# Performance work log

Measured on AMD Instinct MI355X. Metric: run time of the kernel, lower is better.

## Reference

```python
import jax, jax.numpy as jnp
import numpy as np

B, TQ, TK = 2, 2048, 2048
D_IN, D_OUT, H = 1024, 1024, 16
HD = D_OUT // H  # head dim = 64


def setup_inputs() -> dict:
    key = jax.random.key(0)
    ks = jax.random.split(key, 11)
    s = 1.0 / np.sqrt(D_IN)
    so = 1.0 / np.sqrt(D_OUT)
    return {
        "q": jax.random.normal(ks[0], (B, TQ, D_IN), jnp.float32),
        "k": jax.random.normal(ks[1], (B, TK, D_IN), jnp.float32),
        "v": jax.random.normal(ks[2], (B, TK, D_IN), jnp.float32),
        "Wq": jax.random.uniform(ks[3], (D_OUT, D_IN), jnp.float32, -s, s),
        "bq": jax.random.uniform(ks[4], (D_OUT,), jnp.float32, -s, s),
        "Wk": jax.random.uniform(ks[5], (D_OUT, D_IN), jnp.float32, -s, s),
        "bk": jax.random.uniform(ks[6], (D_OUT,), jnp.float32, -s, s),
        "Wv": jax.random.uniform(ks[7], (D_OUT, D_IN), jnp.float32, -s, s),
        "bv": jax.random.uniform(ks[8], (D_OUT,), jnp.float32, -s, s),
        "Wo": jax.random.uniform(ks[9], (D_OUT, D_OUT), jnp.float32, -so, so),
        "bo": jax.random.uniform(ks[10], (D_OUT,), jnp.float32, -so, so),
    }


def reference(q, k, v, Wq, bq, Wk, bk, Wv, bv, Wo, bo):
    b, tq, _ = q.shape
    tk = k.shape[1]
    # linear projections, split heads: [B,T,D] -> [B,H,T,HD]
    qh = (q @ Wq.T + bq).reshape(b, tq, H, HD).transpose(0, 2, 1, 3)
    kh = (k @ Wk.T + bk).reshape(b, tk, H, HD).transpose(0, 2, 1, 3)
    vh = (v @ Wv.T + bv).reshape(b, tk, H, HD).transpose(0, 2, 1, 3)
    # scaled dot-product attention (forward never applies the causal mask)
    scores = jnp.einsum("bhqd,bhkd->bhqk", qh, kh) / np.sqrt(HD).astype(np.float32)
    attn = jax.nn.softmax(scores, axis=-1)
    x = jnp.einsum("bhqk,bhkd->bhqd", attn, vh)
    x = x.transpose(0, 2, 1, 3).reshape(b, tq, D_OUT)
    return x @ Wo.T + bo
```

## Files before the change

kernel.cpp:

```cpp
#include <hip/hip_runtime.h>
#include <hip/hip_bf16.h>

typedef __bf16 b16x8 __attribute__((ext_vector_type(8)));
typedef unsigned short u16x8 __attribute__((ext_vector_type(8)));
typedef unsigned short u16x4 __attribute__((ext_vector_type(4)));
typedef unsigned int u32x4 __attribute__((ext_vector_type(4)));
typedef unsigned int u32x2 __attribute__((ext_vector_type(2)));
typedef float f32x4 __attribute__((ext_vector_type(4)));
typedef float f32x16 __attribute__((ext_vector_type(16)));

__device__ __forceinline__ unsigned short f2b(float f) {
  unsigned u = __builtin_bit_cast(unsigned, f);
  u += 0x7fff + ((u >> 16) & 1);
  return (unsigned short)(u >> 16);
}

__device__ __forceinline__ b16x8 as_b(u16x8 v) { return __builtin_bit_cast(b16x8, v); }

__device__ __forceinline__ float fexp2(float x) {
#if __has_builtin(__builtin_amdgcn_exp2f)
  return __builtin_amdgcn_exp2f(x);
#else
  return exp2f(x);
#endif
}

__device__ __forceinline__ unsigned cvtpk(float lo, float hi) {
  unsigned r;
  asm("v_cvt_pk_bf16_f32 %0, %1, %2" : "=v"(r) : "v"(lo), "v"(hi));
  return r;
}

__device__ __forceinline__ void plswap(unsigned& a, unsigned& b) {
  asm volatile("v_permlane32_swap_b32 %0, %1" : "+v"(a), "+v"(b));
}

__device__ __forceinline__ b16x8 mkchunk(float p0, float p1, float p2, float p3,
                                         float p4, float p5, float p6, float p7) {
  unsigned a1 = cvtpk(p0, p1), b1 = cvtpk(p4, p5);
  unsigned a2 = cvtpk(p2, p3), b2 = cvtpk(p6, p7);
  plswap(a1, b1);
  plswap(a2, b2);
  u32x4 w = {a1, a2, b1, b2};
  return __builtin_bit_cast(b16x8, w);
}

#define AS1 __attribute__((address_space(1)))
#define AS3 __attribute__((address_space(3)))
__device__ __forceinline__ void gload_lds16(const void* g, void* l) {
  __builtin_amdgcn_global_load_lds((const AS1 void*)g, (AS3 void*)l, 16, 0, 0);
}


__global__ __launch_bounds__(256) void convert_kernel(
    const float* __restrict__ q, const float* __restrict__ k, const float* __restrict__ v,
    const float* __restrict__ Wq, const float* __restrict__ Wk,
    const float* __restrict__ Wv, const float* __restrict__ Wo,
    unsigned short* __restrict__ qb, unsigned short* __restrict__ kb,
    unsigned short* __restrict__ vb, unsigned short* __restrict__ wqb,
    unsigned short* __restrict__ wkb, unsigned short* __restrict__ wvb,
    unsigned short* __restrict__ wob) {
  const float* src; unsigned short* dst; int rows;
  switch (blockIdx.y) {
    case 0: src = q;  dst = qb;  rows = 4096; break;
    case 1: src = k;  dst = kb;  rows = 4096; break;
    case 2: src = v;  dst = vb;  rows = 4096; break;
    case 3: src = Wq; dst = wqb; rows = 1024; break;
    case 4: src = Wk; dst = wkb; rows = 1024; break;
    case 5: src = Wv; dst = wvb; rows = 1024; break;
    default: src = Wo; dst = wob; rows = 1024; break;
  }
  const int row = blockIdx.x * 2 + (threadIdx.x >> 7);
  if (row >= rows) return;
  const int t = threadIdx.x & 127;
  const float* sp = src + (size_t)row * 1024 + t * 8;
  float4 f0 = *(const float4*)sp;
  float4 f1 = *(const float4*)(sp + 4);
  u16x8 h = { f2b(f0.x), f2b(f0.y), f2b(f0.z), f2b(f0.w),
              f2b(f1.x), f2b(f1.y), f2b(f1.z), f2b(f1.w) };
  const int swcol = ((t >> 3) << 6) | (((t & 7) ^ (row & 7)) << 3);
  *(u16x8*)(dst + (size_t)row * 1024 + swcol) = h;
}

template <int MODE, typename TOUT>
__device__ __forceinline__ void gemm_body(unsigned short* sA, unsigned short* sB,
                                          const unsigned short* __restrict__ A,
                                          const unsigned short* __restrict__ Bm,
                                          const float* __restrict__ bias,
                                          TOUT* __restrict__ C) {
  const int tid = threadIdx.x;
  const int l = tid & 63, w = tid >> 6;
  const int wm = w >> 1, wn = w & 1;
  const int lr = l & 15, lg = l >> 4;
  const int bm = blockIdx.y * 64, bn = blockIdx.x * 128;
  const int r8 = l >> 3, sl = l & 7;

  f32x4 acc[2][4] = {};

  for (int k0 = 0; k0 < 1024; k0 += 64) {
#pragma unroll
    for (int i = 0; i < 2; ++i) {
      const int row = i * 32 + w * 8 + r8;
      gload_lds16(A + (size_t)(bm + row) * 1024 + k0 + sl * 8, &sA[i * 2048 + w * 512]);
    }
#pragma unroll
    for (int i = 0; i < 4; ++i) {
      const int row = i * 32 + w * 8 + r8;
      gload_lds16(Bm + (size_t)(bn + row) * 1024 + k0 + sl * 8, &sB[i * 2048 + w * 512]);
    }
    __syncthreads();

    b16x8 af[2][2], bf[4][2];
#pragma unroll
    for (int mb = 0; mb < 2; ++mb)
#pragma unroll
      for (int kh = 0; kh < 2; ++kh) {
        const int r = wm * 32 + mb * 16 + lr;
        af[mb][kh] = as_b(*(const u16x8*)(&sA[(r * 64 + kh * 32 + lg * 8) ^ ((r & 7) << 3)]));
      }
#pragma unroll
    for (int nb = 0; nb < 4; ++nb)
#pragma unroll
      for (int kh = 0; kh < 2; ++kh) {
        const int r = wn * 64 + nb * 16 + lr;
        bf[nb][kh] = as_b(*(const u16x8*)(&sB[(r * 64 + kh * 32 + lg * 8) ^ ((r & 7) << 3)]));
      }
#pragma unroll
    for (int mb = 0; mb < 2; ++mb)
#pragma unroll
      for (int nb = 0; nb < 4; ++nb) {
        acc[mb][nb] = __builtin_amdgcn_mfma_f32_16x16x32_bf16(af[mb][0], bf[nb][0], acc[mb][nb], 0, 0, 0);
        acc[mb][nb] = __builtin_amdgcn_mfma_f32_16x16x32_bf16(af[mb][1], bf[nb][1], acc[mb][nb], 0, 0, 0);
      }
    __syncthreads();
  }

  const float qscale = 0.125f * 1.44269504f;
#pragma unroll
  for (int mb = 0; mb < 2; ++mb)
#pragma unroll
    for (int nb = 0; nb < 4; ++nb) {
      const int c = bn + wn * 64 + nb * 16 + lr;
      const float bv = bias[c];
      const int r0 = bm + wm * 32 + mb * 16 + lg * 4;
      if constexpr (MODE == 2) {
        const int hh = c >> 6, hd = c & 63;
        const int bb = r0 >> 11, t0 = r0 & 2047;
        u16x4 pk = { f2b(acc[mb][nb][0] + bv), f2b(acc[mb][nb][1] + bv),
                     f2b(acc[mb][nb][2] + bv), f2b(acc[mb][nb][3] + bv) };
        const int tsw = (t0 & ~63) | (((((t0 >> 3) & 7) ^ (hd & 7)) << 3)) | (t0 & 7);
        *(u16x4*)(&C[(((size_t)bb * 16 + hh) * 64 + hd) * 2048 + tsw]) = pk;
      } else {
#pragma unroll
        for (int i = 0; i < 4; ++i) {
          float val = acc[mb][nb][i] + bv;
          if constexpr (MODE == 1) val *= qscale;
          if constexpr (MODE == 3) {
            C[(size_t)(r0 + i) * 1024 + c] = val;
          } else {
            const int cc = (c & ~63) | (((((c >> 3) & 7) ^ ((r0 + i) & 7)) << 3)) | (c & 7);
            C[(size_t)(r0 + i) * 1024 + cc] = (TOUT)f2b(val);
          }
        }
      }
    }
}

__global__ __launch_bounds__(256) void proj_kernel(
    const unsigned short* __restrict__ qb, const unsigned short* __restrict__ kb,
    const unsigned short* __restrict__ vb,
    const unsigned short* __restrict__ wqb, const float* __restrict__ bq,
    const unsigned short* __restrict__ wkb, const float* __restrict__ bk,
    const unsigned short* __restrict__ wvb, const float* __restrict__ bv,
    unsigned short* __restrict__ Qh, unsigned short* __restrict__ Kh,
    unsigned short* __restrict__ Vt) {
  __shared__ __align__(16) unsigned short sA[64 * 64];
  __shared__ __align__(16) unsigned short sB[128 * 64];
  if (blockIdx.z == 0)      gemm_body<1, unsigned short>(sA, sB, qb, wqb, bq, Qh);
  else if (blockIdx.z == 1) gemm_body<0, unsigned short>(sA, sB, kb, wkb, bk, Kh);
  else                      gemm_body<2, unsigned short>(sA, sB, vb, wvb, bv, Vt);
}

__global__ __launch_bounds__(256) void out_kernel(
    const unsigned short* __restrict__ X, const unsigned short* __restrict__ wob,
    const float* __restrict__ bo, float* __restrict__ out) {
  __shared__ __align__(16) unsigned short sA[64 * 64];
  __shared__ __align__(16) unsigned short sB[128 * 64];
  gemm_body<3, float>(sA, sB, X, wob, bo, out);
}

__global__ __launch_bounds__(256, 2) void attn_kernel(
    const unsigned short* __restrict__ Qh, const unsigned short* __restrict__ Kh,
    const unsigned short* __restrict__ Vt, unsigned short* __restrict__ X) {
  __shared__ __align__(16) unsigned short sK[2][64 * 64];
  __shared__ __align__(16) unsigned short sV[2][64 * 64];

  const int tid = threadIdx.x;
  const int l = tid & 63, wq = tid >> 6;
  const int lq = l & 31, lg = l >> 5;
  const int b = blockIdx.y >> 4, h = blockIdx.y & 15;
  const int q0 = blockIdx.x * 128 + wq * 32;

  const size_t baseQK = (size_t)b * 2048 * 1024 + (size_t)h * 64;
  const size_t baseV  = ((size_t)(b * 16 + h)) * 64 * 2048;

  const int rk = lq & 7;
  b16x8 qf0, qf1, qf2, qf3;
  {
    const unsigned short* qp = Qh + baseQK + (size_t)(q0 + lq) * 1024;
    qf0 = as_b(*(const u16x8*)(qp + (((0 + lg) ^ rk) << 3)));
    qf1 = as_b(*(const u16x8*)(qp + (((2 + lg) ^ rk) << 3)));
    qf2 = as_b(*(const u16x8*)(qp + (((4 + lg) ^ rk) << 3)));
    qf3 = as_b(*(const u16x8*)(qp + (((6 + lg) ^ rk) << 3)));
  }

  const int r8 = l >> 3, sl = l & 7;

  auto stage = [&](int buf, int kv0) {
#pragma unroll
    for (int i = 0; i < 2; ++i) {
      const int rowb = 16 * wq + 8 * i;
      gload_lds16(Kh + baseQK + (size_t)(kv0 + rowb + r8) * 1024 + sl * 8, &sK[buf][rowb * 64]);
      gload_lds16(Vt + baseV + (size_t)(rowb + r8) * 2048 + kv0 + sl * 8, &sV[buf][rowb * 64]);
    }
  };

  float m_run = -1e30f, l_run = 0.f;
  f32x16 Oa = {}, Ob = {};

  stage(0, 0);
  __syncthreads();

  for (int t = 0; t < 32; ++t) {
    const int cur = t & 1;
    if (t + 1 < 32) stage(cur ^ 1, (t + 1) * 64);

    const unsigned short* K_ = sK[cur];
    const unsigned short* V_ = sV[cur];
    const int sw = (lq & 7) << 3;

    f32x16 s0 = {}, s1 = {};
    __builtin_amdgcn_s_setprio(1);
#pragma unroll
    for (int c = 0; c < 4; ++c) {
      const int hd8 = c * 16 + 8 * lg;
      b16x8 kf0 = as_b(*(const u16x8*)(&K_[lq * 64 + (hd8 ^ sw)]));
      b16x8 kf1 = as_b(*(const u16x8*)(&K_[(32 + lq) * 64 + (hd8 ^ sw)]));
      b16x8 qf = (c == 0) ? qf0 : (c == 1) ? qf1 : (c == 2) ? qf2 : qf3;
      s0 = __builtin_amdgcn_mfma_f32_32x32x16_bf16(kf0, qf, s0, 0, 0, 0);
      s1 = __builtin_amdgcn_mfma_f32_32x32x16_bf16(kf1, qf, s1, 0, 0, 0);
    }
    __builtin_amdgcn_s_setprio(0);

    float a0 = fmaxf(fmaxf(s0[0], s0[1]), fmaxf(s0[2], s0[3]));
    float a1 = fmaxf(fmaxf(s0[4], s0[5]), fmaxf(s0[6], s0[7]));
    float a2 = fmaxf(fmaxf(s0[8], s0[9]), fmaxf(s0[10], s0[11]));
    float a3 = fmaxf(fmaxf(s0[12], s0[13]), fmaxf(s0[14], s0[15]));
    float a4 = fmaxf(fmaxf(s1[0], s1[1]), fmaxf(s1[2], s1[3]));
    float a5 = fmaxf(fmaxf(s1[4], s1[5]), fmaxf(s1[6], s1[7]));
    float a6 = fmaxf(fmaxf(s1[8], s1[9]), fmaxf(s1[10], s1[11]));
    float a7 = fmaxf(fmaxf(s1[12], s1[13]), fmaxf(s1[14], s1[15]));
    float mx = fmaxf(fmaxf(fmaxf(a0, a1), fmaxf(a2, a3)),
                     fmaxf(fmaxf(a4, a5), fmaxf(a6, a7)));
    mx = fmaxf(mx, __shfl_xor(mx, 32));

    if (__any(mx > m_run + 8.0f)) {
      const float mnew = fmaxf(m_run, mx);
      const float al = fexp2(m_run - mnew);
      m_run = mnew;
      l_run *= al;
#pragma unroll
      for (int j = 0; j < 16; ++j) { Oa[j] *= al; Ob[j] *= al; }
    }

#pragma unroll
    for (int j = 0; j < 16; ++j) s0[j] = fexp2(s0[j] - m_run);
#pragma unroll
    for (int j = 0; j < 16; ++j) s1[j] = fexp2(s1[j] - m_run);

    float r0 = ((s0[0] + s0[1]) + (s0[2] + s0[3])) + ((s0[4] + s0[5]) + (s0[6] + s0[7]));
    float r1 = ((s0[8] + s0[9]) + (s0[10] + s0[11])) + ((s0[12] + s0[13]) + (s0[14] + s0[15]));
    float r2 = ((s1[0] + s1[1]) + (s1[2] + s1[3])) + ((s1[4] + s1[5]) + (s1[6] + s1[7]));
    float r3 = ((s1[8] + s1[9]) + (s1[10] + s1[11])) + ((s1[12] + s1[13]) + (s1[14] + s1[15]));
    float rs = (r0 + r1) + (r2 + r3);
    rs += __shfl_xor(rs, 32);
    l_run += rs;

    b16x8 pb0 = mkchunk(s0[0], s0[1], s0[2], s0[3], s0[4], s0[5], s0[6], s0[7]);
    b16x8 pb1 = mkchunk(s0[8], s0[9], s0[10], s0[11], s0[12], s0[13], s0[14], s0[15]);
    b16x8 pb2 = mkchunk(s1[0], s1[1], s1[2], s1[3], s1[4], s1[5], s1[6], s1[7]);
    b16x8 pb3 = mkchunk(s1[8], s1[9], s1[10], s1[11], s1[12], s1[13], s1[14], s1[15]);

    __builtin_amdgcn_s_setprio(1);
#pragma unroll
    for (int c = 0; c < 4; ++c) {
      const int kv8 = c * 16 + 8 * lg;
      b16x8 vfa = as_b(*(const u16x8*)(&V_[lq * 64 + (kv8 ^ sw)]));
      b16x8 vfb = as_b(*(const u16x8*)(&V_[(32 + lq) * 64 + (kv8 ^ sw)]));
      b16x8 pb = (c == 0) ? pb0 : (c == 1) ? pb1 : (c == 2) ? pb2 : pb3;
      Oa = __builtin_amdgcn_mfma_f32_32x32x16_bf16(vfa, pb, Oa, 0, 0, 0);
      Ob = __builtin_amdgcn_mfma_f32_32x32x16_bf16(vfb, pb, Ob, 0, 0, 0);
    }
    __builtin_amdgcn_s_setprio(0);
    __syncthreads();
  }

  const float inv = 1.0f / l_run;
  unsigned short* xp = X + baseQK + (size_t)(q0 + lq) * 1024;
#pragma unroll
  for (int g = 0; g < 4; ++g) {
    u32x2 wa = { cvtpk(Oa[4 * g + 0] * inv, Oa[4 * g + 1] * inv),
                 cvtpk(Oa[4 * g + 2] * inv, Oa[4 * g + 3] * inv) };
    *(u32x2*)(xp + ((g ^ rk) << 3) + 4 * lg) = wa;
    u32x2 wb = { cvtpk(Ob[4 * g + 0] * inv, Ob[4 * g + 1] * inv),
                 cvtpk(Ob[4 * g + 2] * inv, Ob[4 * g + 3] * inv) };
    *(u32x2*)(xp + (((4 + g) ^ rk) << 3) + 4 * lg) = wb;
  }
}

extern "C" void kernel_launch(void* const* d_in, const int* in_sizes, int n_in,
                              void* d_out, int out_size, void* d_ws, size_t ws_size,
                              hipStream_t stream) {
  const float* q  = (const float*)d_in[0];
  const float* k  = (const float*)d_in[1];
  const float* v  = (const float*)d_in[2];
  const float* Wq = (const float*)d_in[3];
  const float* bq = (const float*)d_in[4];
  const float* Wk = (const float*)d_in[5];
  const float* bk = (const float*)d_in[6];
  const float* Wv = (const float*)d_in[7];
  const float* bv = (const float*)d_in[8];
  const float* Wo = (const float*)d_in[9];
  const float* bo = (const float*)d_in[10];

  unsigned short* ws = (unsigned short*)d_ws;
  const size_t M1 = (size_t)1024 * 1024;
  unsigned short* qb  = ws;
  unsigned short* kb  = ws + 4 * M1;
  unsigned short* vb  = ws + 8 * M1;
  unsigned short* wqb = ws + 12 * M1;
  unsigned short* wkb = ws + 13 * M1;
  unsigned short* wvb = ws + 14 * M1;
  unsigned short* wob = ws + 15 * M1;
  unsigned short* Qh  = ws + 16 * M1;
  unsigned short* Kh  = ws + 20 * M1;
  unsigned short* Vt  = ws + 24 * M1;
  unsigned short* X   = qb;

  dim3 blk(256);
  convert_kernel<<<dim3(2048, 7), blk, 0, stream>>>(q, k, v, Wq, Wk, Wv, Wo,
                                                    qb, kb, vb, wqb, wkb, wvb, wob);
  proj_kernel<<<dim3(8, 64, 3), blk, 0, stream>>>(qb, kb, vb, wqb, bq, wkb, bk, wvb, bv,
                                                  Qh, Kh, Vt);
  attn_kernel<<<dim3(16, 32), blk, 0, stream>>>(Qh, Kh, Vt, X);
  out_kernel<<<dim3(8, 64), blk, 0, stream>>>(X, wob, bo, (float*)d_out);
}
```

Measured before the change: 138.0 us.

## Split attention KV range across two wave groups per block and merge via LDS

```diff
diff --git a/kernel.cpp b/kernel.cpp
--- a/kernel.cpp
+++ b/kernel.cpp
@@ -189,20 +189,28 @@
   gemm_body<3, float>(sA, sB, X, wob, bo, out);
 }
 
-__global__ __launch_bounds__(256, 2) void attn_kernel(
+__global__ __launch_bounds__(512, 4) void attn_kernel(
     const unsigned short* __restrict__ Qh, const unsigned short* __restrict__ Kh,
     const unsigned short* __restrict__ Vt, unsigned short* __restrict__ X) {
-  __shared__ __align__(16) unsigned short sK[2][64 * 64];
-  __shared__ __align__(16) unsigned short sV[2][64 * 64];
+  __shared__ __align__(16) unsigned short sMem[8][64 * 64];
 
   const int tid = threadIdx.x;
   const int l = tid & 63, wq = tid >> 6;
+  const int half = wq >> 2, w4 = wq & 3;
   const int lq = l & 31, lg = l >> 5;
-  const int b = blockIdx.y >> 4, h = blockIdx.y & 15;
-  const int q0 = blockIdx.x * 128 + wq * 32;
+
+  const int id = blockIdx.x + (int)(gridDim.x * blockIdx.y);
+  const int id2 = (id & 7) * 64 + (id >> 3);
+  const int bx = id2 & 15, by = id2 >> 4;
+  const int b = by >> 4, h = by & 15;
+  const int q0 = bx * 128 + w4 * 32;
+  const int kvbase = half * 1024;
 
   const size_t baseQK = (size_t)b * 2048 * 1024 + (size_t)h * 64;
   const size_t baseV  = ((size_t)(b * 16 + h)) * 64 * 2048;
+
+  unsigned short* sK[2] = { &sMem[half * 4 + 0][0], &sMem[half * 4 + 1][0] };
+  unsigned short* sV[2] = { &sMem[half * 4 + 2][0], &sMem[half * 4 + 3][0] };
 
   const int rk = lq & 7;
   b16x8 qf0, qf1, qf2, qf3;
@@ -219,27 +227,29 @@
   auto stage = [&](int buf, int kv0) {
 #pragma unroll
     for (int i = 0; i < 2; ++i) {
-      const int rowb = 16 * wq + 8 * i;
-      gload_lds16(Kh + baseQK + (size_t)(kv0 + rowb + r8) * 1024 + sl * 8, &sK[buf][rowb * 64]);
-      gload_lds16(Vt + baseV + (size_t)(rowb + r8) * 2048 + kv0 + sl * 8, &sV[buf][rowb * 64]);
+      const int rowb = 16 * w4 + 8 * i;
+      gload_lds16(Kh + baseQK + (size_t)(kv0 + rowb + r8) * 1024 + sl * 8, sK[buf] + rowb * 64);
+      gload_lds16(Vt + baseV + (size_t)(rowb + r8) * 2048 + kv0 + sl * 8, sV[buf] + rowb * 64);
     }
   };
 
-  float m_run = -1e30f, l_run = 0.f;
+  float m_run = 0.f, l_run = 0.f;
   f32x16 Oa = {}, Ob = {};
 
-  stage(0, 0);
+  stage(0, kvbase);
   __syncthreads();
 
-  for (int t = 0; t < 32; ++t) {
+  for (int t = 0; t < 16; ++t) {
     const int cur = t & 1;
-    if (t + 1 < 32) stage(cur ^ 1, (t + 1) * 64);
+    if (t + 1 < 16) stage(cur ^ 1, kvbase + (t + 1) * 64);
 
     const unsigned short* K_ = sK[cur];
     const unsigned short* V_ = sV[cur];
     const int sw = (lq & 7) << 3;
 
-    f32x16 s0 = {}, s1 = {};
+    f32x16 s0, s1;
+#pragma unroll
+    for (int j = 0; j < 16; ++j) { s0[j] = -m_run; s1[j] = -m_run; }
     __builtin_amdgcn_s_setprio(1);
 #pragma unroll
     for (int c = 0; c < 4; ++c) {
@@ -264,19 +274,21 @@
                      fmaxf(fmaxf(a4, a5), fmaxf(a6, a7)));
     mx = fmaxf(mx, __shfl_xor(mx, 32));
 
-    if (__any(mx > m_run + 8.0f)) {
-      const float mnew = fmaxf(m_run, mx);
-      const float al = fexp2(m_run - mnew);
-      m_run = mnew;
+    if (__any(mx > 8.0f)) {
+      const float dm = fmaxf(mx, 0.f);
+      const float al = fexp2(-dm);
+      m_run += dm;
       l_run *= al;
 #pragma unroll
-      for (int j = 0; j < 16; ++j) { Oa[j] *= al; Ob[j] *= al; }
-    }
-
-#pragma unroll
-    for (int j = 0; j < 16; ++j) s0[j] = fexp2(s0[j] - m_run);
-#pragma unroll
-    for (int j = 0; j < 16; ++j) s1[j] = fexp2(s1[j] - m_run);
+      for (int j = 0; j < 16; ++j) {
+        Oa[j] *= al; Ob[j] *= al; s0[j] -= dm; s1[j] -= dm;
+      }
+    }
+
+#pragma unroll
+    for (int j = 0; j < 16; ++j) s0[j] = fexp2(s0[j]);
+#pragma unroll
+    for (int j = 0; j < 16; ++j) s1[j] = fexp2(s1[j]);
 
     float r0 = ((s0[0] + s0[1]) + (s0[2] + s0[3])) + ((s0[4] + s0[5]) + (s0[6] + s0[7]));
     float r1 = ((s0[8] + s0[9]) + (s0[10] + s0[11])) + ((s0[12] + s0[13]) + (s0[14] + s0[15]));
@@ -305,16 +317,38 @@
     __syncthreads();
   }
 
-  const float inv = 1.0f / l_run;
-  unsigned short* xp = X + baseQK + (size_t)(q0 + lq) * 1024;
-#pragma unroll
-  for (int g = 0; g < 4; ++g) {
-    u32x2 wa = { cvtpk(Oa[4 * g + 0] * inv, Oa[4 * g + 1] * inv),
-                 cvtpk(Oa[4 * g + 2] * inv, Oa[4 * g + 3] * inv) };
-    *(u32x2*)(xp + ((g ^ rk) << 3) + 4 * lg) = wa;
-    u32x2 wb = { cvtpk(Ob[4 * g + 0] * inv, Ob[4 * g + 1] * inv),
-                 cvtpk(Ob[4 * g + 2] * inv, Ob[4 * g + 3] * inv) };
-    *(u32x2*)(xp + (((4 + g) ^ rk) << 3) + 4 * lg) = wb;
+  float* fb = (float*)&sMem[0][0];
+  const int mbase = w4 * 64 + l;
+  if (half == 1) {
+    fb[0 * 256 + mbase] = m_run;
+    fb[1 * 256 + mbase] = l_run;
+#pragma unroll
+    for (int j = 0; j < 16; ++j) fb[(2 + j) * 256 + mbase] = Oa[j];
+#pragma unroll
+    for (int j = 0; j < 16; ++j) fb[(18 + j) * 256 + mbase] = Ob[j];
+  }
+  __syncthreads();
+  if (half == 0) {
+    const float m2 = fb[0 * 256 + mbase], l2 = fb[1 * 256 + mbase];
+    const float mM = fmaxf(m_run, m2);
+    const float c1 = fexp2(m_run - mM), c2 = fexp2(m2 - mM);
+    const float inv = 1.0f / (l_run * c1 + l2 * c2);
+    const float ia = c1 * inv, ib = c2 * inv;
+#pragma unroll
+    for (int j = 0; j < 16; ++j) {
+      Oa[j] = Oa[j] * ia + fb[(2 + j) * 256 + mbase] * ib;
+      Ob[j] = Ob[j] * ia + fb[(18 + j) * 256 + mbase] * ib;
+    }
+    unsigned short* xp = X + baseQK + (size_t)(q0 + lq) * 1024;
+#pragma unroll
+    for (int g = 0; g < 4; ++g) {
+      u32x2 wa = { cvtpk(Oa[4 * g + 0], Oa[4 * g + 1]),
+                   cvtpk(Oa[4 * g + 2], Oa[4 * g + 3]) };
+      *(u32x2*)(xp + ((g ^ rk) << 3) + 4 * lg) = wa;
+      u32x2 wb = { cvtpk(Ob[4 * g + 0], Ob[4 * g + 1]),
+                   cvtpk(Ob[4 * g + 2], Ob[4 * g + 3]) };
+      *(u32x2*)(xp + (((4 + g) ^ rk) << 3) + 4 * lg) = wb;
+    }
   }
 }
 
@@ -352,6 +386,6 @@
                                                     qb, kb, vb, wqb, wkb, wvb, wob);
   proj_kernel<<<dim3(8, 64, 3), blk, 0, stream>>>(qb, kb, vb, wqb, bq, wkb, bk, wvb, bv,
                                                   Qh, Kh, Vt);
-  attn_kernel<<<dim3(16, 32), blk, 0, stream>>>(Qh, Kh, Vt, X);
+  attn_kernel<<<dim3(16, 32), dim3(512), 0, stream>>>(Qh, Kh, Vt, X);
   out_kernel<<<dim3(8, 64), blk, 0, stream>>>(X, wob, bo, (float*)d_out);
 }
```

New measurement: 177.1 us. 1.28x slower.
